# Kernel optimization log

Measured on AMD Instinct MI355X. Metric: run time of the kernel, lower is better.

The kernel has to match this reference:

```python
import jax, jax.numpy as jnp
import numpy as np

N_NODES = 10000
N_EDGES = 200000
N_GRAPHS = 500
HID = 256            # hidden_dim*2 inside E3GNN with hidden_dim=128
NUM_FREQS = 10
DIS_DIM = NUM_FREQS * 2 * 3  # 60
EDGE_IN = 2 * HID + 9 + DIS_DIM  # 581


def setup_inputs() -> dict:
    key = jax.random.key(0)
    ks = jax.random.split(key, 16)
    inp = {
        "node_features": jax.random.normal(ks[0], (N_NODES, HID), dtype=jnp.float32),
        "frac_coords": jax.random.uniform(ks[1], (N_NODES, 3), dtype=jnp.float32),
        "lattices": jax.random.normal(ks[2], (N_GRAPHS, 3, 3), dtype=jnp.float32),
        "edge_index": jax.random.randint(ks[3], (2, N_EDGES), 0, N_NODES, dtype=jnp.int64),
        "edge2graph": jax.random.randint(ks[4], (N_EDGES,), 0, N_GRAPHS, dtype=jnp.int64),
    }
    def lin(k, fan_in, fan_out):
        bound = 1.0 / np.sqrt(fan_in)
        kw, kb = jax.random.split(k)
        W = jax.random.uniform(kw, (fan_in, fan_out), minval=-bound, maxval=bound, dtype=jnp.float32)
        b = jax.random.uniform(kb, (fan_out,), minval=-bound, maxval=bound, dtype=jnp.float32)
        return W, b
    inp["We1"], inp["be1"] = lin(ks[5], EDGE_IN, HID)
    inp["We2"], inp["be2"] = lin(ks[6], HID, HID)
    inp["Wn1"], inp["bn1"] = lin(ks[7], 2 * HID, HID)
    inp["Wn2"], inp["bn2"] = lin(ks[8], HID, HID)
    return inp


def reference(node_features, frac_coords, lattices, edge_index, edge2graph,
              We1, be1, We2, be2, Wn1, bn1, Wn2, bn2):
    src, dst = edge_index[0], edge_index[1]
    E = src.shape[0]
    N = node_features.shape[0]

    # --- edge model ---
    hi = node_features[src]                      # [E, H]
    hj = node_features[dst]                      # [E, H]
    frac_diff = jnp.mod(frac_coords[dst] - frac_coords[src], 1.0)  # [E, 3]
    # SinusoidsEmbedding
    freqs = 2.0 * jnp.pi * jnp.arange(NUM_FREQS, dtype=frac_diff.dtype)
    emb = (frac_diff[:, :, None] * freqs).reshape(E, 3 * NUM_FREQS)  # [E, 30]
    dis = jnp.concatenate([jnp.sin(emb), jnp.cos(emb)], axis=-1)     # [E, 60]
    # lattice inner products, gathered per edge
    lat_ips = jnp.einsum('gij,gkj->gik', lattices, lattices).reshape(-1, 9)[edge2graph]  # [E, 9]

    e_in = jnp.concatenate([hi, hj, lat_ips, dis], axis=-1)          # [E, 581]
    e = jax.nn.silu(e_in @ We1 + be1)
    e = jax.nn.silu(e @ We2 + be2)                                   # [E, H]

    # --- node model: scatter-mean over source index ---
    agg = jax.ops.segment_sum(e, src, num_segments=N)                # [N, H]
    cnt = jax.ops.segment_sum(jnp.ones((E,), e.dtype), src, num_segments=N)
    agg = agg / jnp.maximum(cnt, 1.0)[:, None]

    n_in = jnp.concatenate([node_features, agg], axis=-1)            # [N, 2H]
    out = jax.nn.silu(n_in @ Wn1 + bn1)
    out = jax.nn.silu(out @ Wn2 + bn2)

    return node_features + out
```

## Files before the change

kernel.cpp:

```cpp
#include <hip/hip_runtime.h>
#include <hip/hip_bf16.h>
#include <stdint.h>

#define E_N    200000
#define NODES  10000
#define GRAPHS 500
#define HID    256
#define K1RAW  581
#define K1P    640

typedef short bf16x8 __attribute__((ext_vector_type(8)));
typedef float f32x4  __attribute__((ext_vector_type(4)));

__device__ __forceinline__ short f2bf(float f){
  uint32_t u = __float_as_uint(f);
  u = (u + 0x7fffu + ((u >> 16) & 1u)) >> 16;
  return (short)u;
}
__device__ __forceinline__ float silu_f(float x){ return x / (1.f + __expf(-x)); }

__device__ __forceinline__ void pack_one(const float* __restrict__ W, short* __restrict__ Wp,
                                         int K, int idx){
  int lane = idx & 63, t = idx >> 6;
  int nb = t & 15, kb = t >> 4;
  int n  = nb * 16 + (lane & 15);
  int k0 = kb * 32 + ((lane >> 4) << 3);
  bf16x8 v;
#pragma unroll
  for (int j = 0; j < 8; ++j){
    int k = k0 + j;
    v[j] = (k < K) ? f2bf(W[k * HID + n]) : (short)0;
  }
  ((bf16x8*)Wp)[idx] = v;
}

__global__ void prep_kernel(const float* __restrict__ We1, const float* __restrict__ We2,
                            const float* __restrict__ Wn1, const float* __restrict__ Wn2,
                            const float* __restrict__ nf, const float* __restrict__ lattices,
                            const int* __restrict__ ei,
                            short* We1p, short* We2p, short* Wn1p, short* Wn2p,
                            short* nfb, float* latw, float* cnt)
{
  int idx = blockIdx.x * 256 + threadIdx.x;
  if (idx < 20480){ pack_one(We1, We1p, K1RAW, idx); return; }
  idx -= 20480;
  if (idx < 8192){ pack_one(We2, We2p, HID, idx); return; }
  idx -= 8192;
  if (idx < 16384){ pack_one(Wn1, Wn1p, 512, idx); return; }
  idx -= 16384;
  if (idx < 8192){ pack_one(Wn2, Wn2p, HID, idx); return; }
  idx -= 8192;
  if (idx < 320000){
    const f32x4* p = (const f32x4*)(nf + (size_t)idx * 8);
    f32x4 a = p[0], b = p[1];
    bf16x8 v;
#pragma unroll
    for (int j = 0; j < 4; ++j){ v[j] = f2bf(a[j]); v[4+j] = f2bf(b[j]); }
    ((bf16x8*)nfb)[idx] = v;
    return;
  }
  idx -= 320000;
  if (idx < 4500){
    int g = idx / 9, r = idx % 9, i = r / 3, k = r % 3;
    const float* L = lattices + g * 9;
    latw[idx] = L[i*3+0]*L[k*3+0] + L[i*3+1]*L[k*3+1] + L[i*3+2]*L[k*3+2];
    return;
  }
  idx -= 4500;
  if (idx < E_N){
    atomicAdd(&cnt[ei[idx]], 1.f);
  }
}

__global__ __launch_bounds__(512) void edge_kernel(
    const int* __restrict__ ei, const float* __restrict__ fc,
    const float* __restrict__ latw, const int* __restrict__ e2g,
    const short* __restrict__ nfb,
    const short* __restrict__ We1p, const short* __restrict__ We2p,
    const float* __restrict__ be1, const float* __restrict__ be2,
    float* __restrict__ agg)
{
  __shared__ short A_s[64][72];
  __shared__ short H1_s[64][264];
  __shared__ int   src_s[64];
  __shared__ int   dst_s[64];
  __shared__ float fd_s[64][3];
  __shared__ float lat_s[64][9];

  const int tid = threadIdx.x;
  const int e0  = blockIdx.x * 64;

  if (tid < 64){
    int e = e0 + tid;
    int s = ei[e], d = ei[E_N + e];
    src_s[tid] = s; dst_s[tid] = d;
    int g = e2g[e];
#pragma unroll
    for (int c = 0; c < 3; ++c){
      float df = fc[d*3+c] - fc[s*3+c];
      fd_s[tid][c] = df - floorf(df);
    }
#pragma unroll
    for (int j = 0; j < 9; ++j) lat_s[tid][j] = latw[g*9+j];
  }
  __syncthreads();

  const int lane = tid & 63;
  const int w    = tid >> 6;
  const int r    = tid >> 3;
  const int cg   = tid & 7;
  const int arow = lane & 15;
  const int koff = (lane >> 4) << 3;
  const int rbase = (lane >> 4) << 2;
  const int colbase = w*32 + arow;

  const f32x4 zero4 = {0.f, 0.f, 0.f, 0.f};
  f32x4 acc[4][2];
#pragma unroll
  for (int i = 0; i < 4; ++i){ acc[i][0] = zero4; acc[i][1] = zero4; }

  auto stage_val = [&](int kc) -> bf16x8 {
    bf16x8 v;
    if (kc < 8){
      int node = (kc < 4) ? src_s[r] : dst_s[r];
      v = *(const bf16x8*)(nfb + (size_t)node * HID + (kc & 3) * 64 + cg * 8);
    } else {
#pragma unroll
      for (int j = 0; j < 8; ++j){
        int k = kc * 64 + cg * 8 + j;
        float val = 0.f;
        if (k < 521){
          val = lat_s[r][k - 512];
        } else if (k < 581){
          int m = k - 521;
          int mm = (m < 30) ? m : (m - 30);
          int coord = mm / 10, q = mm - coord * 10;
          float ang = 6.283185307179586f * (float)q * fd_s[r][coord];
          val = (m < 30) ? __sinf(ang) : __cosf(ang);
        }
        v[j] = f2bf(val);
      }
    }
    return v;
  };

  bf16x8 stg = stage_val(0);
#pragma unroll
  for (int kc = 0; kc < 10; ++kc){
    __syncthreads();
    *(bf16x8*)&A_s[r][cg*8] = stg;
    if (kc < 9) stg = stage_val(kc + 1);
    __syncthreads();
#pragma unroll
    for (int sub = 0; sub < 2; ++sub){
      const int kb = kc*2 + sub;
      bf16x8 b0 = ((const bf16x8*)We1p)[(kb*16 + w*2 + 0)*64 + lane];
      bf16x8 b1 = ((const bf16x8*)We1p)[(kb*16 + w*2 + 1)*64 + lane];
#pragma unroll
      for (int rf = 0; rf < 4; ++rf){
        bf16x8 a = *(const bf16x8*)&A_s[rf*16 + arow][sub*32 + koff];
        acc[rf][0] = __builtin_amdgcn_mfma_f32_16x16x32_bf16(a, b0, acc[rf][0], 0, 0, 0);
        acc[rf][1] = __builtin_amdgcn_mfma_f32_16x16x32_bf16(a, b1, acc[rf][1], 0, 0, 0);
      }
    }
  }

  float b1c0 = be1[colbase], b1c1 = be1[colbase + 16];
#pragma unroll
  for (int rf = 0; rf < 4; ++rf){
#pragma unroll
    for (int j = 0; j < 4; ++j){
      int row = rf*16 + rbase + j;
      H1_s[row][colbase]      = f2bf(silu_f(acc[rf][0][j] + b1c0));
      H1_s[row][colbase + 16] = f2bf(silu_f(acc[rf][1][j] + b1c1));
    }
  }
  __syncthreads();

  f32x4 acc2[4][2];
#pragma unroll
  for (int i = 0; i < 4; ++i){ acc2[i][0] = zero4; acc2[i][1] = zero4; }
#pragma unroll
  for (int kb = 0; kb < 8; ++kb){
    bf16x8 b0 = ((const bf16x8*)We2p)[(kb*16 + w*2 + 0)*64 + lane];
    bf16x8 b1 = ((const bf16x8*)We2p)[(kb*16 + w*2 + 1)*64 + lane];
#pragma unroll
    for (int rf = 0; rf < 4; ++rf){
      bf16x8 a = *(const bf16x8*)&H1_s[rf*16 + arow][kb*32 + koff];
      acc2[rf][0] = __builtin_amdgcn_mfma_f32_16x16x32_bf16(a, b0, acc2[rf][0], 0, 0, 0);
      acc2[rf][1] = __builtin_amdgcn_mfma_f32_16x16x32_bf16(a, b1, acc2[rf][1], 0, 0, 0);
    }
  }

  float b2c0 = be2[colbase], b2c1 = be2[colbase + 16];
#pragma unroll
  for (int rf = 0; rf < 4; ++rf){
#pragma unroll
    for (int j = 0; j < 4; ++j){
      int row = rf*16 + rbase + j;
      int s = src_s[row];
      atomicAdd(&agg[(size_t)s*HID + colbase],      silu_f(acc2[rf][0][j] + b2c0));
      atomicAdd(&agg[(size_t)s*HID + colbase + 16], silu_f(acc2[rf][1][j] + b2c1));
    }
  }
}

__global__ __launch_bounds__(512) void node_kernel(
    const short* __restrict__ nfb, const float* __restrict__ agg,
    const float* __restrict__ cnt,
    const short* __restrict__ Wn1p, const short* __restrict__ Wn2p,
    const float* __restrict__ bn1, const float* __restrict__ bn2,
    const float* __restrict__ nf, float* __restrict__ out)
{
  __shared__ short A_s[64][72];
  __shared__ short H1_s[64][264];
  __shared__ float rinv_s[64];

  const int tid = threadIdx.x;
  const int r0  = blockIdx.x * 64;
  if (tid < 64){
    int row = r0 + tid;
    float c = (row < NODES) ? cnt[row] : 1.f;
    rinv_s[tid] = 1.f / fmaxf(c, 1.f);
  }
  __syncthreads();

  const int lane = tid & 63;
  const int w    = tid >> 6;
  const int r    = tid >> 3;
  const int cg   = tid & 7;
  const int arow = lane & 15;
  const int koff = (lane >> 4) << 3;
  const int rbase = (lane >> 4) << 2;
  const int colbase = w*32 + arow;
  const int grow = min(r0 + r, NODES - 1);

  const f32x4 zero4 = {0.f, 0.f, 0.f, 0.f};
  f32x4 acc[4][2];
#pragma unroll
  for (int i = 0; i < 4; ++i){ acc[i][0] = zero4; acc[i][1] = zero4; }

  auto stage_val = [&](int kc) -> bf16x8 {
    bf16x8 v;
    if (kc < 4){
      v = *(const bf16x8*)(nfb + (size_t)grow * HID + kc*64 + cg*8);
    } else {
      const float* p = agg + (size_t)grow * HID + (kc - 4)*64 + cg*8;
      f32x4 a = *(const f32x4*)p, b = *(const f32x4*)(p + 4);
      float s = rinv_s[r];
#pragma unroll
      for (int j = 0; j < 4; ++j){ v[j] = f2bf(a[j]*s); v[4+j] = f2bf(b[j]*s); }
    }
    return v;
  };

  bf16x8 stg = stage_val(0);
#pragma unroll
  for (int kc = 0; kc < 8; ++kc){
    __syncthreads();
    *(bf16x8*)&A_s[r][cg*8] = stg;
    if (kc < 7) stg = stage_val(kc + 1);
    __syncthreads();
#pragma unroll
    for (int sub = 0; sub < 2; ++sub){
      const int kb = kc*2 + sub;
      bf16x8 b0 = ((const bf16x8*)Wn1p)[(kb*16 + w*2 + 0)*64 + lane];
      bf16x8 b1 = ((const bf16x8*)Wn1p)[(kb*16 + w*2 + 1)*64 + lane];
#pragma unroll
      for (int rf = 0; rf < 4; ++rf){
        bf16x8 a = *(const bf16x8*)&A_s[rf*16 + arow][sub*32 + koff];
        acc[rf][0] = __builtin_amdgcn_mfma_f32_16x16x32_bf16(a, b0, acc[rf][0], 0, 0, 0);
        acc[rf][1] = __builtin_amdgcn_mfma_f32_16x16x32_bf16(a, b1, acc[rf][1], 0, 0, 0);
      }
    }
  }

  float b1c0 = bn1[colbase], b1c1 = bn1[colbase + 16];
#pragma unroll
  for (int rf = 0; rf < 4; ++rf){
#pragma unroll
    for (int j = 0; j < 4; ++j){
      int row = rf*16 + rbase + j;
      H1_s[row][colbase]      = f2bf(silu_f(acc[rf][0][j] + b1c0));
      H1_s[row][colbase + 16] = f2bf(silu_f(acc[rf][1][j] + b1c1));
    }
  }
  __syncthreads();

  f32x4 acc2[4][2];
#pragma unroll
  for (int i = 0; i < 4; ++i){ acc2[i][0] = zero4; acc2[i][1] = zero4; }
#pragma unroll
  for (int kb = 0; kb < 8; ++kb){
    bf16x8 b0 = ((const bf16x8*)Wn2p)[(kb*16 + w*2 + 0)*64 + lane];
    bf16x8 b1 = ((const bf16x8*)Wn2p)[(kb*16 + w*2 + 1)*64 + lane];
#pragma unroll
    for (int rf = 0; rf < 4; ++rf){
      bf16x8 a = *(const bf16x8*)&H1_s[rf*16 + arow][kb*32 + koff];
      acc2[rf][0] = __builtin_amdgcn_mfma_f32_16x16x32_bf16(a, b0, acc2[rf][0], 0, 0, 0);
      acc2[rf][1] = __builtin_amdgcn_mfma_f32_16x16x32_bf16(a, b1, acc2[rf][1], 0, 0, 0);
    }
  }

  float b2c0 = bn2[colbase], b2c1 = bn2[colbase + 16];
#pragma unroll
  for (int rf = 0; rf < 4; ++rf){
#pragma unroll
    for (int j = 0; j < 4; ++j){
      int row = rf*16 + rbase + j;
      int grw = r0 + row;
      if (grw < NODES){
        size_t o0 = (size_t)grw * HID + colbase;
        out[o0]      = silu_f(acc2[rf][0][j] + b2c0) + nf[o0];
        out[o0 + 16] = silu_f(acc2[rf][1][j] + b2c1) + nf[o0 + 16];
      }
    }
  }
}

extern "C" void kernel_launch(void* const* d_in, const int* in_sizes, int n_in,
                              void* d_out, int out_size, void* d_ws, size_t ws_size,
                              hipStream_t stream) {
  const float* nf       = (const float*)d_in[0];
  const float* fc       = (const float*)d_in[1];
  const float* lattices = (const float*)d_in[2];
  const int*   ei       = (const int*)d_in[3];
  const int*   e2g      = (const int*)d_in[4];
  const float* We1      = (const float*)d_in[5];
  const float* be1      = (const float*)d_in[6];
  const float* We2      = (const float*)d_in[7];
  const float* be2      = (const float*)d_in[8];
  const float* Wn1      = (const float*)d_in[9];
  const float* bn1      = (const float*)d_in[10];
  const float* Wn2      = (const float*)d_in[11];
  const float* bn2      = (const float*)d_in[12];
  float* out = (float*)d_out;

  char* ws = (char*)d_ws;
  float* agg  = (float*)(ws);
  float* cnt  = (float*)(ws + 10240000);
  short* nfb  = (short*)(ws + 10280000);
  float* latw = (float*)(ws + 15400000);
  short* We1p = (short*)(ws + 15418000);
  short* We2p = (short*)(ws + 15745680);
  short* Wn1p = (short*)(ws + 15876752);
  short* Wn2p = (short*)(ws + 16138896);

  hipMemsetAsync(ws, 0, 10280000, stream);

  prep_kernel<<<2257, 256, 0, stream>>>(We1, We2, Wn1, Wn2, nf, lattices, ei,
                                        We1p, We2p, Wn1p, Wn2p, nfb, latw, cnt);

  edge_kernel<<<E_N / 64, 512, 0, stream>>>(ei, fc, latw, e2g, nfb, We1p, We2p,
                                            be1, be2, agg);

  node_kernel<<<(NODES + 63) / 64, 512, 0, stream>>>(nfb, agg, cnt, Wn1p, Wn2p,
                                                     bn1, bn2, nf, out);
}
```

Measured before the change: 343.3 us.

## Sort edges by source via counting sort and pre-reduce atomics per run

Adds a single-block prefix scan over per-node counts and a bucketing kernel that builds a permutation grouping edges by source node. The edge kernel then processes edges in that order and merges consecutive rows sharing a source within each 4-row fragment before issuing atomicAdds, cutting atomic traffic and contention on agg. In exchange it adds two kernel launches, a serial single-block scan, and an indirect gather through perm that makes the reads of ei, e2g and fc less coalesced. Edge order within a bucket is nondeterministic, so float summation order varies between runs.

```diff
diff --git a/kernel.cpp b/kernel.cpp
--- a/kernel.cpp
+++ b/kernel.cpp
@@ -72,9 +72,48 @@
   }
 }
 
+__global__ __launch_bounds__(1024) void scan_kernel(const float* __restrict__ cnt,
+                                                    int* __restrict__ cursor)
+{
+  __shared__ int part[1024];
+  const int t = threadIdx.x;
+  const int base = t * 10;
+  int v[10]; int s = 0;
+#pragma unroll
+  for (int k = 0; k < 10; ++k){
+    int idx = base + k;
+    int c = (idx < NODES) ? (int)cnt[idx] : 0;
+    v[k] = c; s += c;
+  }
+  part[t] = s; __syncthreads();
+  for (int off = 1; off < 1024; off <<= 1){
+    int add = (t >= off) ? part[t - off] : 0;
+    __syncthreads();
+    part[t] += add; __syncthreads();
+  }
+  int run = part[t] - s;
+#pragma unroll
+  for (int k = 0; k < 10; ++k){
+    int idx = base + k;
+    if (idx < NODES){ cursor[idx] = run; run += v[k]; }
+  }
+}
+
+__global__ void bucket_kernel(const int* __restrict__ ei, int* __restrict__ cursor,
+                              int* __restrict__ perm)
+{
+  int e = blockIdx.x * 256 + threadIdx.x;
+  if (e < E_N){
+    int s = ei[e];
+    int pos = atomicAdd(&cursor[s], 1);
+    perm[pos] = e;
+  }
+}
+
 __global__ __launch_bounds__(512) void edge_kernel(
     const int* __restrict__ ei, const float* __restrict__ fc,
     const float* __restrict__ latw, const int* __restrict__ e2g,
+    const int* __restrict__ perm,
     const short* __restrict__ nfb,
     const short* __restrict__ We1p, const short* __restrict__ We2p,
     const float* __restrict__ be1, const float* __restrict__ be2,
@@ -91,7 +130,7 @@
   const int e0  = blockIdx.x * 64;
 
   if (tid < 64){
-    int e = e0 + tid;
+    int e = perm[e0 + tid];
     int s = ei[e], d = ei[E_N + e];
     src_s[tid] = s; dst_s[tid] = d;
     int g = e2g[e];
@@ -195,13 +234,24 @@
   float b2c0 = be2[colbase], b2c1 = be2[colbase + 16];
 #pragma unroll
   for (int rf = 0; rf < 4; ++rf){
-#pragma unroll
-    for (int j = 0; j < 4; ++j){
-      int row = rf*16 + rbase + j;
-      int s = src_s[row];
-      atomicAdd(&agg[(size_t)s*HID + colbase],      silu_f(acc2[rf][0][j] + b2c0));
-      atomicAdd(&agg[(size_t)s*HID + colbase + 16], silu_f(acc2[rf][1][j] + b2c1));
-    }
+    const int rrow = rf*16 + rbase;
+    int   cur  = src_s[rrow];
+    float run0 = silu_f(acc2[rf][0][0] + b2c0);
+    float run1 = silu_f(acc2[rf][1][0] + b2c1);
+#pragma unroll
+    for (int j = 1; j < 4; ++j){
+      int   s2 = src_s[rrow + j];
+      float w0 = silu_f(acc2[rf][0][j] + b2c0);
+      float w1 = silu_f(acc2[rf][1][j] + b2c1);
+      if (s2 == cur){ run0 += w0; run1 += w1; }
+      else {
+        atomicAdd(&agg[(size_t)cur*HID + colbase],      run0);
+        atomicAdd(&agg[(size_t)cur*HID + colbase + 16], run1);
+        cur = s2; run0 = w0; run1 = w1;
+      }
+    }
+    atomicAdd(&agg[(size_t)cur*HID + colbase],      run0);
+    atomicAdd(&agg[(size_t)cur*HID + colbase + 16], run1);
   }
 }
 
@@ -337,22 +387,28 @@
   float* out = (float*)d_out;
 
   char* ws = (char*)d_ws;
-  float* agg  = (float*)(ws);
-  float* cnt  = (float*)(ws + 10240000);
-  short* nfb  = (short*)(ws + 10280000);
-  float* latw = (float*)(ws + 15400000);
-  short* We1p = (short*)(ws + 15418000);
-  short* We2p = (short*)(ws + 15745680);
-  short* Wn1p = (short*)(ws + 15876752);
-  short* Wn2p = (short*)(ws + 16138896);
+  float* agg    = (float*)(ws);
+  float* cnt    = (float*)(ws + 10240000);
+  short* nfb    = (short*)(ws + 10280000);
+  float* latw   = (float*)(ws + 15400000);
+  short* We1p   = (short*)(ws + 15418000);
+  short* We2p   = (short*)(ws + 15745680);
+  short* Wn1p   = (short*)(ws + 15876752);
+  short* Wn2p   = (short*)(ws + 16138896);
+  int*   cursor = (int*)  (ws + 16269968);
+  int*   perm   = (int*)  (ws + 16309968);
 
   hipMemsetAsync(ws, 0, 10280000, stream);
 
   prep_kernel<<<2257, 256, 0, stream>>>(We1, We2, Wn1, Wn2, nf, lattices, ei,
                                         We1p, We2p, Wn1p, Wn2p, nfb, latw, cnt);
 
-  edge_kernel<<<E_N / 64, 512, 0, stream>>>(ei, fc, latw, e2g, nfb, We1p, We2p,
-                                            be1, be2, agg);
+  scan_kernel<<<1, 1024, 0, stream>>>(cnt, cursor);
+
+  bucket_kernel<<<(E_N + 255) / 256, 256, 0, stream>>>(ei, cursor, perm);
+
+  edge_kernel<<<E_N / 64, 512, 0, stream>>>(ei, fc, latw, e2g, perm, nfb,
+                                            We1p, We2p, be1, be2, agg);
 
   node_kernel<<<(NODES + 63) / 64, 512, 0, stream>>>(nfb, agg, cnt, Wn1p, Wn2p,
                                                      bn1, bn2, nf, out);
```

After: 362.0 us. 1.05x slower.
